# Performance work log

Hardware: AMD Instinct MI355X
Metric: run time of the kernel (lower is better)

The kernel has to match this reference:

```python
import jax, jax.numpy as jnp
import numpy as np


def setup_inputs() -> dict:
    key = jax.random.key(0)
    kx, ky = jax.random.split(key)
    N, D = 8192, 128
    x = jax.random.normal(kx, (N, D), dtype=jnp.float32)
    y = jax.random.normal(ky, (N, D), dtype=jnp.float32)
    return {"x": x, "y": y}


def reference(x, y):
    # L2 contrastive loss (Kostic et al. 2024, NCP):
    #   1/(N(N-1)) * sum_{i != j} <x_i, y_j>^2  -  2/N * sum_i <x_i, y_i>
    N = x.shape[0]
    K = x @ y.T                      # (N, N) pairwise dot products
    diag = jnp.diagonal(K)           # <x_i, y_i>
    off_diag_sq = jnp.sum(K * K) - jnp.sum(diag * diag)
    loss = off_diag_sq / (N * (N - 1)) - 2.0 / N * jnp.sum(diag)
    return loss
```

## Files before the change

kernel.cpp:

```cpp
#include <hip/hip_runtime.h>

#define DD 128
#define SR 72
#define PP 128
#define NB (2*PP)

typedef float f32x4 __attribute__((ext_vector_type(4)));
typedef short s16x8 __attribute__((ext_vector_type(8)));

__global__ __launch_bounds__(512)
void gram_kernel(const float* __restrict__ x, const float* __restrict__ y,
                 float* __restrict__ apart, float* __restrict__ bpart,
                 double* __restrict__ ds1, double* __restrict__ ds2, int N)
{
  const int blk = blockIdx.x;
  const bool isX = blk < PP;
  const int p = isX ? blk : blk - PP;
  const float* __restrict__ src = isX ? x : y;
  const int slab = N / PP;
  const int row0 = p * slab;

  __shared__ __align__(16) unsigned short sh_hi[DD * SR];
  __shared__ __align__(16) unsigned short sh_lo[DD * SR];
  __shared__ double wred[8][2];

  const int tid = threadIdx.x;
  const int wave = tid >> 6, lane = tid & 63;
  const int rloc = tid >> 3;
  const int fg = tid & 7;

  f32x4 acc[8];
#pragma unroll
  for (int t = 0; t < 8; ++t)
#pragma unroll
    for (int k = 0; k < 4; ++k) acc[t][k] = 0.f;

  double s1 = 0.0, s2 = 0.0;

  {
    const float* cb = src + (size_t)row0 * DD;
    const float4* rowp = (const float4*)(cb + rloc * DD);
    float4 v0 = rowp[fg], v1 = rowp[fg + 8], v2 = rowp[fg + 16], v3 = rowp[fg + 24];

    if (isX) {
      const float4* yrp = (const float4*)(y + (size_t)row0 * DD + rloc * DD);
      float4 w0 = yrp[fg], w1 = yrp[fg + 8], w2 = yrp[fg + 16], w3 = yrp[fg + 24];
      float d = v0.x*w0.x + v0.y*w0.y + v0.z*w0.z + v0.w*w0.w
              + v1.x*w1.x + v1.y*w1.y + v1.z*w1.z + v1.w*w1.w
              + v2.x*w2.x + v2.y*w2.y + v2.z*w2.z + v2.w*w2.w
              + v3.x*w3.x + v3.y*w3.y + v3.z*w3.z + v3.w*w3.w;
      d += __shfl_down(d, 4, 8);
      d += __shfl_down(d, 2, 8);
      d += __shfl_down(d, 1, 8);
      if (fg == 0) { s1 += (double)d; s2 += (double)d * (double)d; }
    }

    {
      float vals[16] = {v0.x, v0.y, v0.z, v0.w, v1.x, v1.y, v1.z, v1.w,
                        v2.x, v2.y, v2.z, v2.w, v3.x, v3.y, v3.z, v3.w};
#pragma unroll
      for (int j = 0; j < 4; ++j)
#pragma unroll
        for (int cc = 0; cc < 4; ++cc) {
          const int m = ((fg + (j << 3)) << 2) + cc;
          const float vv = vals[j * 4 + cc];
          const unsigned int b = __float_as_uint(vv);
          const unsigned short hb = (unsigned short)(b >> 16);
          const float hf = __uint_as_float(b & 0xffff0000u);
          const float lf = vv - hf;
          const unsigned short lb = (unsigned short)(__float_as_uint(lf) >> 16);
          sh_hi[m * SR + rloc] = hb;
          sh_lo[m * SR + rloc] = lb;
        }
    }
    __syncthreads();

#pragma unroll
    for (int kb = 0; kb < 64; kb += 32) {
      const int ko = kb + ((lane >> 4) << 3);
      const int arow = (wave * 16 + (lane & 15)) * SR + ko;
      const s16x8 ahi = *(const s16x8*)&sh_hi[arow];
      const s16x8 alo = *(const s16x8*)&sh_lo[arow];
#pragma unroll
      for (int t = 0; t < 8; ++t) {
        const int brow = (t * 16 + (lane & 15)) * SR + ko;
        const s16x8 bhi = *(const s16x8*)&sh_hi[brow];
        const s16x8 blo = *(const s16x8*)&sh_lo[brow];
        acc[t] = __builtin_amdgcn_mfma_f32_16x16x32_bf16(ahi, bhi, acc[t], 0, 0, 0);
        acc[t] = __builtin_amdgcn_mfma_f32_16x16x32_bf16(ahi, blo, acc[t], 0, 0, 0);
        acc[t] = __builtin_amdgcn_mfma_f32_16x16x32_bf16(alo, bhi, acc[t], 0, 0, 0);
      }
    }
  }

  f32x4* __restrict__ dst4 = (f32x4*)((isX ? apart : bpart) + (size_t)p * (DD * DD));
#pragma unroll
  for (int t = 0; t < 8; ++t)
    dst4[t * 512 + tid] = acc[t];

  if (isX) {
    s1 += __shfl_down(s1, 32, 64); s2 += __shfl_down(s2, 32, 64);
    s1 += __shfl_down(s1, 16, 64); s2 += __shfl_down(s2, 16, 64);
    s1 += __shfl_down(s1, 8, 64);  s2 += __shfl_down(s2, 8, 64);
    if (lane == 0) { wred[wave][0] = s1; wred[wave][1] = s2; }
    __syncthreads();
    if (tid == 0) {
      double t1 = 0.0, t2 = 0.0;
#pragma unroll
      for (int g = 0; g < 8; ++g) { t1 += wred[g][0]; t2 += wred[g][1]; }
      ds1[p] = t1;
      ds2[p] = t2;
    }
  }
}

__global__ __launch_bounds__(256)
void dot_kernel(const float* __restrict__ apart, const float* __restrict__ bpart,
                double* __restrict__ prod)
{
  const int tid = threadIdx.x;
  const int s = tid & 15;
  const int pg = tid >> 4;
  const f32x4* __restrict__ a4 = (const f32x4*)apart;
  const f32x4* __restrict__ b4 = (const f32x4*)bpart;
  const int base = blockIdx.x * 16 + s;

  f32x4 sa = {0.f, 0.f, 0.f, 0.f}, sb = {0.f, 0.f, 0.f, 0.f};
#pragma unroll
  for (int i = 0; i < 8; ++i) {
    const int p = pg + (i << 4);
    sa += a4[(size_t)p * (DD * DD / 4) + base];
    sb += b4[(size_t)p * (DD * DD / 4) + base];
  }

  __shared__ f32x4 sA[16][16], sB[16][16];
  sA[pg][s] = sa;
  sB[pg][s] = sb;
  __syncthreads();

  if (tid < 16) {
    f32x4 ta = sA[0][tid], tb = sB[0][tid];
#pragma unroll
    for (int g = 1; g < 16; ++g) { ta += sA[g][tid]; tb += sB[g][tid]; }
    double pr = (double)ta[0] * (double)tb[0]
              + (double)ta[1] * (double)tb[1]
              + (double)ta[2] * (double)tb[2]
              + (double)ta[3] * (double)tb[3];
    pr += __shfl_down(pr, 8, 16);
    pr += __shfl_down(pr, 4, 16);
    pr += __shfl_down(pr, 2, 16);
    pr += __shfl_down(pr, 1, 16);
    if (tid == 0) prod[blockIdx.x] = pr;
  }
}

__global__ __launch_bounds__(256)
void finish_kernel(const double* __restrict__ prod,
                   const double* __restrict__ ds1, const double* __restrict__ ds2,
                   float* __restrict__ out, int N)
{
  const int tid = threadIdx.x;
  const int wv = tid >> 6, lane = tid & 63;
  __shared__ double red[4][3];

  double S = prod[tid];
  double t1 = (tid < PP) ? ds1[tid] : 0.0;
  double t2 = (tid < PP) ? ds2[tid] : 0.0;
#pragma unroll
  for (int off = 32; off > 0; off >>= 1) {
    S  += __shfl_down(S, off, 64);
    t1 += __shfl_down(t1, off, 64);
    t2 += __shfl_down(t2, off, 64);
  }
  if (lane == 0) { red[wv][0] = S; red[wv][1] = t1; red[wv][2] = t2; }
  __syncthreads();
  if (tid == 0) {
    double Sf = red[0][0] + red[1][0] + red[2][0] + red[3][0];
    double d1 = red[0][1] + red[1][1] + red[2][1] + red[3][1];
    double d2 = red[0][2] + red[1][2] + red[2][2] + red[3][2];
    double loss = (Sf - d2) / ((double)N * (double)(N - 1)) - (2.0 / N) * d1;
    out[0] = (float)loss;
  }
}

extern "C" void kernel_launch(void* const* d_in, const int* in_sizes, int n_in,
                              void* d_out, int out_size, void* d_ws, size_t ws_size,
                              hipStream_t stream) {
  const float* x = (const float*)d_in[0];
  const float* y = (const float*)d_in[1];
  float* out = (float*)d_out;
  const int N = in_sizes[0] / DD;

  char* w = (char*)d_ws;
  float* apart = (float*)w;                              w += (size_t)PP * DD * DD * 4;
  float* bpart = (float*)w;                              w += (size_t)PP * DD * DD * 4;
  double* ds1  = (double*)w;                             w += PP * 8;
  double* ds2  = (double*)w;                             w += PP * 8;
  double* prod = (double*)w;

  gram_kernel<<<NB, 512, 0, stream>>>(x, y, apart, bpart, ds1, ds2, N);
  dot_kernel<<<(DD * DD) / 64, 256, 0, stream>>>(apart, bpart, prod);
  finish_kernel<<<1, 256, 0, stream>>>(prod, ds1, ds2, out, N);
}
```

Baseline: 71.81 us.

## Exploit Gram symmetry: compute only upper-triangular 16x16 tiles

Since X^T X and Y^T Y are symmetric, only the 36 upper-triangular 16x16 tiles of each 128x128 Gram matrix are computed, spread across 8 waves (4 or 5 tiles each). Off-diagonal tiles are weighted by 2 in the Frobenius dot product, selected through a bitmask of diagonal tile indices. This cuts MFMA work and partial-matrix traffic by roughly 44%, at the cost of uneven per-wave load and an index mapping computed at runtime.

```diff
diff --git a/kernel.cpp b/kernel.cpp
--- a/kernel.cpp
+++ b/kernel.cpp
@@ -4,6 +4,7 @@
 #define SR 72
 #define PP 128
 #define NB (2*PP)
+#define NT 36
 
 typedef float f32x4 __attribute__((ext_vector_type(4)));
 typedef short s16x8 __attribute__((ext_vector_type(8)));
@@ -29,9 +30,22 @@
   const int rloc = tid >> 3;
   const int fg = tid & 7;
 
-  f32x4 acc[8];
-#pragma unroll
-  for (int t = 0; t < 8; ++t)
+  const int start = (9 * wave) >> 1;
+  const int cnt = 4 + (wave & 1);
+  int tr_[5], tc_[5];
+#pragma unroll
+  for (int j = 0; j < 5; ++j) {
+    const int tile = start + j;
+    int r = 0;
+#pragma unroll
+    for (int q = 1; q < 8; ++q) r += (tile >= ((q * (17 - q)) >> 1)) ? 1 : 0;
+    tr_[j] = r;
+    tc_[j] = tile - ((r * (17 - r)) >> 1) + r;
+  }
+
+  f32x4 acc[5];
+#pragma unroll
+  for (int t = 0; t < 5; ++t)
 #pragma unroll
     for (int k = 0; k < 4; ++k) acc[t][k] = 0.f;
 
@@ -76,27 +90,29 @@
     __syncthreads();
 
 #pragma unroll
-    for (int kb = 0; kb < 64; kb += 32) {
-      const int ko = kb + ((lane >> 4) << 3);
-      const int arow = (wave * 16 + (lane & 15)) * SR + ko;
-      const s16x8 ahi = *(const s16x8*)&sh_hi[arow];
-      const s16x8 alo = *(const s16x8*)&sh_lo[arow];
-#pragma unroll
-      for (int t = 0; t < 8; ++t) {
-        const int brow = (t * 16 + (lane & 15)) * SR + ko;
-        const s16x8 bhi = *(const s16x8*)&sh_hi[brow];
-        const s16x8 blo = *(const s16x8*)&sh_lo[brow];
-        acc[t] = __builtin_amdgcn_mfma_f32_16x16x32_bf16(ahi, bhi, acc[t], 0, 0, 0);
-        acc[t] = __builtin_amdgcn_mfma_f32_16x16x32_bf16(ahi, blo, acc[t], 0, 0, 0);
-        acc[t] = __builtin_amdgcn_mfma_f32_16x16x32_bf16(alo, bhi, acc[t], 0, 0, 0);
+    for (int j = 0; j < 5; ++j) {
+      if (j < cnt) {
+        const int ar0 = (tr_[j] * 16 + (lane & 15)) * SR;
+        const int br0 = (tc_[j] * 16 + (lane & 15)) * SR;
+#pragma unroll
+        for (int kb = 0; kb < 64; kb += 32) {
+          const int ko = kb + ((lane >> 4) << 3);
+          const s16x8 ahi = *(const s16x8*)&sh_hi[ar0 + ko];
+          const s16x8 alo = *(const s16x8*)&sh_lo[ar0 + ko];
+          const s16x8 bhi = *(const s16x8*)&sh_hi[br0 + ko];
+          const s16x8 blo = *(const s16x8*)&sh_lo[br0 + ko];
+          acc[j] = __builtin_amdgcn_mfma_f32_16x16x32_bf16(ahi, bhi, acc[j], 0, 0, 0);
+          acc[j] = __builtin_amdgcn_mfma_f32_16x16x32_bf16(ahi, blo, acc[j], 0, 0, 0);
+          acc[j] = __builtin_amdgcn_mfma_f32_16x16x32_bf16(alo, bhi, acc[j], 0, 0, 0);
+        }
       }
     }
   }
 
-  f32x4* __restrict__ dst4 = (f32x4*)((isX ? apart : bpart) + (size_t)p * (DD * DD));
-#pragma unroll
-  for (int t = 0; t < 8; ++t)
-    dst4[t * 512 + tid] = acc[t];
+  f32x4* __restrict__ dst4 = (f32x4*)(isX ? apart : bpart) + (size_t)p * (NT * 64);
+#pragma unroll
+  for (int j = 0; j < 5; ++j)
+    if (j < cnt) dst4[(start + j) * 64 + lane] = acc[j];
 
   if (isX) {
     s1 += __shfl_down(s1, 32, 64); s2 += __shfl_down(s2, 32, 64);
@@ -129,8 +145,8 @@
 #pragma unroll
   for (int i = 0; i < 8; ++i) {
     const int p = pg + (i << 4);
-    sa += a4[(size_t)p * (DD * DD / 4) + base];
-    sb += b4[(size_t)p * (DD * DD / 4) + base];
+    sa += a4[(size_t)p * (NT * 64) + base];
+    sb += b4[(size_t)p * (NT * 64) + base];
   }
 
   __shared__ f32x4 sA[16][16], sB[16][16];
@@ -142,10 +158,12 @@
     f32x4 ta = sA[0][tid], tb = sB[0][tid];
 #pragma unroll
     for (int g = 1; g < 16; ++g) { ta += sA[g][tid]; tb += sB[g][tid]; }
-    double pr = (double)ta[0] * (double)tb[0]
-              + (double)ta[1] * (double)tb[1]
-              + (double)ta[2] * (double)tb[2]
-              + (double)ta[3] * (double)tb[3];
+    const int tile = (blockIdx.x * 16 + tid) >> 6;
+    const double w = ((0xA44208101ULL >> tile) & 1) ? 1.0 : 2.0;
+    double pr = w * ((double)ta[0] * (double)tb[0]
+                   + (double)ta[1] * (double)tb[1]
+                   + (double)ta[2] * (double)tb[2]
+                   + (double)ta[3] * (double)tb[3]);
     pr += __shfl_down(pr, 8, 16);
     pr += __shfl_down(pr, 4, 16);
     pr += __shfl_down(pr, 2, 16);
@@ -163,7 +181,7 @@
   const int wv = tid >> 6, lane = tid & 63;
   __shared__ double red[4][3];
 
-  double S = prod[tid];
+  double S = (tid < (NT * 64 * 4) / 64) ? prod[tid] : 0.0;
   double t1 = (tid < PP) ? ds1[tid] : 0.0;
   double t2 = (tid < PP) ? ds2[tid] : 0.0;
 #pragma unroll
@@ -192,13 +210,13 @@
   const int N = in_sizes[0] / DD;
 
   char* w = (char*)d_ws;
-  float* apart = (float*)w;                              w += (size_t)PP * DD * DD * 4;
-  float* bpart = (float*)w;                              w += (size_t)PP * DD * DD * 4;
+  float* apart = (float*)w;                              w += (size_t)PP * NT * 256 * 4;
+  float* bpart = (float*)w;                              w += (size_t)PP * NT * 256 * 4;
   double* ds1  = (double*)w;                             w += PP * 8;
   double* ds2  = (double*)w;                             w += PP * 8;
   double* prod = (double*)w;
 
   gram_kernel<<<NB, 512, 0, stream>>>(x, y, apart, bpart, ds1, ds2, N);
-  dot_kernel<<<(DD * DD) / 64, 256, 0, stream>>>(apart, bpart, prod);
+  dot_kernel<<<(NT * 64) / 16, 256, 0, stream>>>(apart, bpart, prod);
   finish_kernel<<<1, 256, 0, stream>>>(prod, ds1, ds2, out, N);
 }
```

Measured after the change: 68.98 us. 1.04x faster.
